# Optimization experiments

Hardware: AMD Instinct MI355X
Metric: run time of the kernel (lower is better)

## Reference

```python
import jax, jax.numpy as jnp
import numpy as np

N_HIDDEN = 512

def _lstm_cell(x, h, c, W_ih, W_hh, b):
    # PyTorch LSTMCell: gates ordered i, f, g, o
    gates = x @ W_ih.T + h @ W_hh.T + b  # [B, 4H]
    i, f, g, o = jnp.split(gates, 4, axis=-1)
    i = jax.nn.sigmoid(i)
    f = jax.nn.sigmoid(f)
    g = jnp.tanh(g)
    o = jax.nn.sigmoid(o)
    c_new = f * c + i * g
    h_new = o * jnp.tanh(c_new)
    return h_new, c_new

def setup_inputs() -> dict:
    key = jax.random.key(0)
    ks = jax.random.split(key, 10)
    B, T, H = 256, 1024, N_HIDDEN
    s1 = 1.0 / np.sqrt(H)
    inp = {
        'x': jax.random.normal(ks[0], (B, T), dtype=jnp.float32),
        'W_ih1': jax.random.uniform(ks[1], (4 * H, 1), jnp.float32, -s1, s1),
        'W_hh1': jax.random.uniform(ks[2], (4 * H, H), jnp.float32, -s1, s1),
        'b1': jax.random.uniform(ks[3], (4 * H,), jnp.float32, -s1, s1),
        'W_ih2': jax.random.uniform(ks[4], (4 * H, H), jnp.float32, -s1, s1),
        'W_hh2': jax.random.uniform(ks[5], (4 * H, H), jnp.float32, -s1, s1),
        'b2': jax.random.uniform(ks[6], (4 * H,), jnp.float32, -s1, s1),
        'W_lin': jax.random.uniform(ks[7], (1, H), jnp.float32, -s1, s1),
        'b_lin': jax.random.uniform(ks[8], (1,), jnp.float32, -s1, s1),
    }
    return inp

def reference(x, W_ih1, W_hh1, b1, W_ih2, W_hh2, b2, W_lin, b_lin):
    B, T = x.shape
    H = W_hh1.shape[1]
    zeros = jnp.zeros((B, H), dtype=x.dtype)
    init = (zeros, zeros, zeros, zeros)
    xs = x.T[:, :, None]  # [T, B, 1]

    def step(carry, x_t):
        h1, c1, h2, c2 = carry
        h1, c1 = _lstm_cell(x_t, h1, c1, W_ih1, W_hh1, b1)
        h2, c2 = _lstm_cell(h1, h2, c2, W_ih2, W_hh2, b2)
        out = h2 @ W_lin.T + b_lin  # [B, 1]
        return (h1, c1, h2, c2), out

    _, outs = jax.lax.scan(step, init, xs)  # outs: [T, B, 1]
    return outs[:, :, 0].T  # [B, T]
```

## Files before the change

### kernel.cpp

```cpp
#include <hip/hip_runtime.h>
#include <math.h>

#define BB   256
#define TT   1024
#define HH   512
#define NWG  256
#define NTHR 512
#define SLOT (HH*BB)
#define PADX 20

typedef _Float16 f16;
typedef _Float16 f16x8 __attribute__((ext_vector_type(8)));
typedef float    f32x4 __attribute__((ext_vector_type(4)));
typedef unsigned int u32;
typedef u32 u32x2 __attribute__((ext_vector_type(2)));
typedef unsigned short u16;
typedef unsigned char u8;

__device__ __forceinline__ f32x4 mf(f16x8 a, f16x8 b, f32x4 c){
  return __builtin_amdgcn_mfma_f32_16x16x32_f16(a, b, c, 0, 0, 0);
}

__device__ __forceinline__ float fast_sigmoid(float v){
  float e = __expf(-v);
  return __builtin_amdgcn_rcpf(1.0f + e);
}
__device__ __forceinline__ float fast_tanh(float v){
  float a = fabsf(v);
  float e = __expf(-2.0f * a);
  float r = (1.0f - e) * __builtin_amdgcn_rcpf(1.0f + e);
  return copysignf(r, v);
}

__device__ __forceinline__ void split_h(float hv, u16& hb, u8& lb){
  const f16 hh = (f16)hv;
  const f16 lh = (f16)((hv - (float)hh) * 2048.0f);
  union {f16 f; u16 u;} ch, cl; ch.f = hh; cl.f = lh;
  hb = ch.u;
  lb = (u8)(((u32)cl.u + 0x80u) >> 8);
}
__device__ __forceinline__ float join_h(u16 hb, u8 lb){
  union {u16 u; f16 f;} h, l;
  h.u = hb; l.u = (u16)((u32)lb << 8);
  return (float)h.f + (float)l.f * (1.0f/2048.0f);
}
__device__ __forceinline__ void st_wt_u16(u16* p, u16 v){
  __hip_atomic_store(p, v, __ATOMIC_RELAXED, __HIP_MEMORY_SCOPE_AGENT);
}
__device__ __forceinline__ void st_wt_u8(u8* p, u8 v){
  __hip_atomic_store(p, v, __ATOMIC_RELAXED, __HIP_MEMORY_SCOPE_AGENT);
}
__device__ __forceinline__ void st_wt_f32(float* p, float v){
  __hip_atomic_store(p, v, __ATOMIC_RELAXED, __HIP_MEMORY_SCOPE_AGENT);
}

__device__ __forceinline__ void build_hl(const u16* ph_, const u8* pl_, f16x8& fh, f16x8& fl){
  union {u32x2 d; u32 u[2];} ha, hb2;
  ha.d  = *(const u32x2*)ph_;
  hb2.d = *(const u32x2*)(ph_ + 1024);
  const u32 l0 = *(const u32*)pl_;
  const u32 l1 = *(const u32*)(pl_ + 1024);
  union {u32 u[4]; f16x8 f;} H, L;
  H.u[0]=ha.u[0]; H.u[1]=ha.u[1]; H.u[2]=hb2.u[0]; H.u[3]=hb2.u[1];
  L.u[0] = __builtin_amdgcn_perm(l0, 0u, 0x05010400u);
  L.u[1] = __builtin_amdgcn_perm(l0, 0u, 0x07010600u);
  L.u[2] = __builtin_amdgcn_perm(l1, 0u, 0x05010400u);
  L.u[3] = __builtin_amdgcn_perm(l1, 0u, 0x07010600u);
  fh = H.f; fl = L.f;
}

__device__ __forceinline__ void gridbar_g(unsigned* barb, unsigned ph){
  __syncthreads();
  if (threadIdx.x == 0){
    __builtin_amdgcn_fence(__ATOMIC_RELEASE, "agent");
    const unsigned g = blockIdx.x & 31u;
    unsigned old = __hip_atomic_fetch_add(&barb[g*16], 1u, __ATOMIC_RELAXED, __HIP_MEMORY_SCOPE_AGENT);
    if (old + 1u == 8u*ph){
      unsigned om = __hip_atomic_fetch_add(&barb[512], 1u, __ATOMIC_RELAXED, __HIP_MEMORY_SCOPE_AGENT);
      if (om + 1u == 32u*ph){
        #pragma unroll
        for (int r = 0; r < 32; ++r)
          __hip_atomic_store(&barb[544 + r*16], ph, __ATOMIC_RELAXED, __HIP_MEMORY_SCOPE_AGENT);
      }
    }
    while (__hip_atomic_load(&barb[544 + g*16], __ATOMIC_RELAXED, __HIP_MEMORY_SCOPE_AGENT) < ph){
      __builtin_amdgcn_s_sleep(2);
    }
    __builtin_amdgcn_fence(__ATOMIC_ACQUIRE, "agent");
  }
  __syncthreads();
}

__global__ __launch_bounds__(NTHR, 2) void lstm_mfma(
    const float* __restrict__ x,      const float* __restrict__ W_ih1,
    const float* __restrict__ W_hh1,  const float* __restrict__ b1,
    const float* __restrict__ W_ih2,  const float* __restrict__ W_hh2,
    const float* __restrict__ b2,     const float* __restrict__ W_lin,
    const float* __restrict__ b_lin,  float* __restrict__ out,
    char* __restrict__ wsb)
{
  __shared__ f16x8 A2hi[2048], A2lo[2048], A1hi[1024], A1lo[1024];
  __shared__ float xch[8][16*PADX];
  __shared__ float wlin_s[512];
  __shared__ float outpart[2][8];

  unsigned* bar = (unsigned*)wsb;
  float* xT = (float*)(wsb + 16384);
  u16* h1h = (u16*)(wsb + 16384 + 1048576);
  u8*  h1l = (u8*) ((char*)h1h + 4*SLOT);
  u16* h2h = (u16*)((char*)h1l + 2*SLOT);
  u8*  h2l = (u8*) ((char*)h2h + 4*SLOT);

  const int w   = blockIdx.x,  tid = threadIdx.x;
  const int l   = tid & 63,    wv  = tid >> 6;
  const int quad = l >> 4,     lc  = l & 15;
  const int p = w >> 1, cb = w & 1;
  const int j0 = 4*p;
  const int bcol = cb*128 + wv*16 + lc;
  const int jq = j0 + quad;
  const int b_out = cb*128 + p;
  unsigned* dbar = bar + cb*1024;
  unsigned* gbar = bar + 2048;
  const unsigned grp = (unsigned)(p >> 3);
  const int qrot = p & 3;

  {
    const int g_ = lc >> 2, jj_ = lc & 3;
    const int wrow = g_*HH + j0 + jj_;
    const float* rowI  = W_ih2 + (size_t)wrow*HH;
    const float* rowH2 = W_hh2 + (size_t)wrow*HH;
    const float* rowH1 = W_hh1 + (size_t)wrow*HH;
    for (int c = wv; c < 32; c += 8){
      const int kb = c*32 + quad*8;
      union {f16x8 v; f16 e[8];} hi8, lo8;
      #pragma unroll
      for (int i = 0; i < 8; ++i){
        const int k = kb + i;
        const float wval = (k < HH) ? rowI[k] : rowH2[k - HH];
        const f16 h_ = (f16)wval;
        hi8.e[i] = h_;
        lo8.e[i] = (f16)((wval - (float)h_) * 2048.0f);
      }
      A2hi[c*64 + l] = hi8.v;
      A2lo[c*64 + l] = lo8.v;
    }
    for (int c = wv; c < 16; c += 8){
      const int kb = c*32 + quad*8;
      union {f16x8 v; f16 e[8];} hi8, lo8;
      #pragma unroll
      for (int i = 0; i < 8; ++i){
        const float wval = rowH1[kb + i];
        const f16 h_ = (f16)wval;
        hi8.e[i] = h_;
        lo8.e[i] = (f16)((wval - (float)h_) * 2048.0f);
      }
      A1hi[c*64 + l] = hi8.v;
      A1lo[c*64 + l] = lo8.v;
    }
  }
  float wih1r[4], b1r[4], b2r[4];
  #pragma unroll
  for (int g = 0; g < 4; ++g){
    wih1r[g] = W_ih1[g*HH + jq];
    b1r[g]   = b1[g*HH + jq];
    b2r[g]   = b2[g*HH + jq];
  }
  const float blin = b_lin[0];
  wlin_s[tid] = W_lin[tid];

  {
    const int gid = w*NTHR + tid;
    #pragma unroll
    for (int i2 = 0; i2 < 2; ++i2){
      const int idx = gid + i2*131072;
      const int bb2 = idx >> 10, tt2 = idx & (TT-1);
      xT[(size_t)tt2*BB + bb2] = x[idx];
    }
  }
  {
    const int idx = w >> 1;
    const int off = SLOT + idx*1024 + (cb*128 + (tid & 127))*4 + (tid >> 7);
    st_wt_u16(&h2h[off], (u16)0);
    st_wt_u8 (&h2l[off], (u8)0);
  }

  gridbar_g(gbar, 1);

  float c1, c2 = 0.0f;
  {
    const float xv0 = xT[bcol];
    const float gi = fast_sigmoid(fmaf(xv0, wih1r[0], b1r[0]));
    const float gg = fast_tanh   (fmaf(xv0, wih1r[2], b1r[2]));
    const float go = fast_sigmoid(fmaf(xv0, wih1r[3], b1r[3]));
    c1 = gi * gg;
    const float hv = go * fast_tanh(c1);
    u16 hb; u8 lb; split_h(hv, hb, lb);
    const int off = p*1024 + bcol*4 + quad;
    st_wt_u16(&h1h[off], hb);
    st_wt_u8 (&h1l[off], lb);
  }
  gridbar_g(gbar, 2);

  for (int t = 0; t < TT; ++t){
    const int sR1 = ( t    & 1)*SLOT;
    const int sR2 = ((t+1) & 1)*SLOT;
    const int sW1 = ((t+1) & 1)*SLOT;
    const int sW2 = ( t    & 1)*SLOT;

    f32x4 aA2 = {0,0,0,0}, aB2 = {0,0,0,0}, aA1 = {0,0,0,0}, aB1 = {0,0,0,0};
    const u16* q1h = h1h + sR1 + quad*2048 + bcol*4;
    const u8*  q1l = h1l + sR1 + quad*2048 + bcol*4;
    const u16* q2h = h2h + sR2 + quad*2048 + bcol*4;
    const u8*  q2l = h2l + sR2 + quad*2048 + bcol*4;

    auto consume_chunk = [&](int c){
      f16x8 bh, bl;
      build_hl(q1h + c*8192, q1l + c*8192, bh, bl);
      const f16x8 a2h = A2hi[c*64 + l];
      const f16x8 a2l = A2lo[c*64 + l];
      const f16x8 a1h = A1hi[c*64 + l];
      const f16x8 a1l = A1lo[c*64 + l];
      aA2 = mf(a2h, bh, aA2);
      aB2 = mf(a2h, bl, aB2);
      aB2 = mf(a2l, bh, aB2);
      aA1 = mf(a1h, bh, aA1);
      aB1 = mf(a1h, bl, aB1);
      aB1 = mf(a1l, bh, aB1);
      f16x8 ch, cl;
      build_hl(q2h + c*8192, q2l + c*8192, ch, cl);
      const f16x8 d2h = A2hi[(c+16)*64 + l];
      const f16x8 d2l = A2lo[(c+16)*64 + l];
      aA2 = mf(d2h, ch, aA2);
      aB2 = mf(d2h, cl, aB2);
      aB2 = mf(d2l, ch, aB2);
    };

    const unsigned need = 8u * (unsigned)t;
    auto poll_mask = [&]() -> unsigned {
      unsigned cv = __hip_atomic_load(&dbar[(l & 15) * 16], __ATOMIC_RELAXED, __HIP_MEMORY_SCOPE_AGENT);
      return (unsigned)__ballot(cv >= need) & 0xFFFFu;
    };

    unsigned got = 0xFFFFu;
    if (t > 0) got = poll_mask();
    asm volatile("" ::: "memory");
    if (got == 0xFFFFu){
      #pragma unroll
      for (int i = 0; i < 16; ++i) consume_chunk((i + 4*qrot) & 15);
    } else {
      #pragma unroll
      for (int q = 0; q < 4; ++q){
        const int c0 = ((qrot + q) & 3) * 4;
        const unsigned qm = 0xFu << c0;
        while ((got & qm) != qm){
          __builtin_amdgcn_s_sleep(1);
          got |= poll_mask();
        }
        asm volatile("" ::: "memory");
        consume_chunk(c0 + 0);
        consume_chunk(c0 + 1);
        consume_chunk(c0 + 2);
        consume_chunk(c0 + 3);
      }
    }
    asm volatile("" ::: "memory");

    const int oidx = sR2 + (tid>>2)*1024 + b_out*4 + (tid&3);
    float opart = join_h(h2h[oidx], h2l[oidx]) * wlin_s[tid];

    float* xw = &xch[wv][0];
    {
      f32x4 pre;
      #pragma unroll
      for (int i = 0; i < 4; ++i) pre[i] = fmaf(aB2[i], 1.0f/2048.0f, aA2[i]);
      *(f32x4*)&xw[lc*PADX + quad*4] = pre;
      __threadfence_block();
      const float g0 = xw[lc*PADX + 0*4 + quad];
      const float g1 = xw[lc*PADX + 1*4 + quad];
      const float g2 = xw[lc*PADX + 2*4 + quad];
      const float g3 = xw[lc*PADX + 3*4 + quad];
      const float gi = fast_sigmoid(g0 + b2r[0]);
      const float gf = fast_sigmoid(g1 + b2r[1]);
      const float gg = fast_tanh   (g2 + b2r[2]);
      const float go = fast_sigmoid(g3 + b2r[3]);
      c2 = fmaf(gf, c2, gi*gg);
      const float hv = go * fast_tanh(c2);
      u16 hb; u8 lb; split_h(hv, hb, lb);
      const int off = sW2 + p*1024 + bcol*4 + quad;
      st_wt_u16(&h2h[off], hb);
      st_wt_u8 (&h2l[off], lb);
    }
    {
      f32x4 pre;
      #pragma unroll
      for (int i = 0; i < 4; ++i) pre[i] = fmaf(aB1[i], 1.0f/2048.0f, aA1[i]);
      __threadfence_block();
      *(f32x4*)&xw[lc*PADX + quad*4] = pre;
      __threadfence_block();
      const float g0 = xw[lc*PADX + 0*4 + quad];
      const float g1 = xw[lc*PADX + 1*4 + quad];
      const float g2 = xw[lc*PADX + 2*4 + quad];
      const float g3 = xw[lc*PADX + 3*4 + quad];
      const int tx = (t+1 < TT) ? (t+1) : (TT-1);
      const float xv = xT[(size_t)tx*BB + bcol];
      const float gi = fast_sigmoid(g0 + fmaf(xv, wih1r[0], b1r[0]));
      const float gf = fast_sigmoid(g1 + fmaf(xv, wih1r[1], b1r[1]));
      const float gg = fast_tanh   (g2 + fmaf(xv, wih1r[2], b1r[2]));
      const float go = fast_sigmoid(g3 + fmaf(xv, wih1r[3], b1r[3]));
      c1 = fmaf(gf, c1, gi*gg);
      const float hv = go * fast_tanh(c1);
      u16 hb; u8 lb; split_h(hv, hb, lb);
      const int off = sW1 + p*1024 + bcol*4 + quad;
      st_wt_u16(&h1h[off], hb);
      st_wt_u8 (&h1l[off], lb);
    }
    #pragma unroll
    for (int off = 32; off > 0; off >>= 1) opart += __shfl_down(opart, off, 64);
    if (l == 0) outpart[t & 1][wv] = opart;

    __syncthreads();
    if (tid == 0){
      __builtin_amdgcn_fence(__ATOMIC_RELEASE, "workgroup");
      __hip_atomic_fetch_add(&dbar[grp*16], 1u, __ATOMIC_RELAXED, __HIP_MEMORY_SCOPE_AGENT);
      __builtin_amdgcn_fence(__ATOMIC_ACQUIRE, "agent");
      if (t > 0){
        float s = blin;
        #pragma unroll
        for (int q2i = 0; q2i < 8; ++q2i) s += outpart[t & 1][q2i];
        st_wt_f32(&out[(size_t)b_out*TT + (t-1)], s);
      }
    }
    __syncthreads();
  }

  {
    const unsigned needT = 8u * (unsigned)TT;
    unsigned gotT = (unsigned)__ballot(
        __hip_atomic_load(&dbar[(l & 15) * 16], __ATOMIC_RELAXED, __HIP_MEMORY_SCOPE_AGENT) >= needT) & 0xFFFFu;
    while (gotT != 0xFFFFu){
      __builtin_amdgcn_s_sleep(1);
      gotT |= (unsigned)__ballot(
          __hip_atomic_load(&dbar[(l & 15) * 16], __ATOMIC_RELAXED, __HIP_MEMORY_SCOPE_AGENT) >= needT) & 0xFFFFu;
    }
    asm volatile("" ::: "memory");

    const int oidx = ((TT-1)&1)*SLOT + (tid>>2)*1024 + b_out*4 + (tid&3);
    float opart = join_h(h2h[oidx], h2l[oidx]) * wlin_s[tid];
    #pragma unroll
    for (int off = 32; off > 0; off >>= 1) opart += __shfl_down(opart, off, 64);
    if (l == 0) outpart[0][wv] = opart;
    __syncthreads();
    if (tid == 0){
      float s = blin;
      #pragma unroll
      for (int q2i = 0; q2i < 8; ++q2i) s += outpart[0][q2i];
      st_wt_f32(&out[(size_t)b_out*TT + (TT-1)], s);
    }
  }
}

extern "C" void kernel_launch(void* const* d_in, const int* in_sizes, int n_in,
                              void* d_out, int out_size, void* d_ws, size_t ws_size,
                              hipStream_t stream) {
  const float* x     = (const float*)d_in[0];
  const float* W_ih1 = (const float*)d_in[1];
  const float* W_hh1 = (const float*)d_in[2];
  const float* b1    = (const float*)d_in[3];
  const float* W_ih2 = (const float*)d_in[4];
  const float* W_hh2 = (const float*)d_in[5];
  const float* b2    = (const float*)d_in[6];
  const float* W_lin = (const float*)d_in[7];
  const float* b_lin = (const float*)d_in[8];
  float* out = (float*)d_out;
  char* wsb  = (char*)d_ws;

  hipMemsetAsync(d_ws, 0, 16384, stream);

  hipLaunchKernelGGL(lstm_mfma, dim3(NWG), dim3(NTHR), 0, stream,
                     x, W_ih1, W_hh1, b1, W_ih2, W_hh2, b2, W_lin, b_lin, out, wsb);
}
```

Before: 12.70 ms.

## Widen hidden-state layout and software-pipeline chunk loads ahead of MFMA compute

```diff
diff --git a/kernel.cpp b/kernel.cpp
--- a/kernel.cpp
+++ b/kernel.cpp
@@ -14,6 +14,7 @@
 typedef float    f32x4 __attribute__((ext_vector_type(4)));
 typedef unsigned int u32;
 typedef u32 u32x2 __attribute__((ext_vector_type(2)));
+typedef u32 u32x4 __attribute__((ext_vector_type(4)));
 typedef unsigned short u16;
 typedef unsigned char u8;
 
@@ -54,20 +55,17 @@
   __hip_atomic_store(p, v, __ATOMIC_RELAXED, __HIP_MEMORY_SCOPE_AGENT);
 }
 
-__device__ __forceinline__ void build_hl(const u16* ph_, const u8* pl_, f16x8& fh, f16x8& fl){
-  union {u32x2 d; u32 u[2];} ha, hb2;
-  ha.d  = *(const u32x2*)ph_;
-  hb2.d = *(const u32x2*)(ph_ + 1024);
-  const u32 l0 = *(const u32*)pl_;
-  const u32 l1 = *(const u32*)(pl_ + 1024);
+__device__ __forceinline__ void build2(u32x4 hd, u32x2 ld2, f16x8& fh, f16x8& fl){
   union {u32 u[4]; f16x8 f;} H, L;
-  H.u[0]=ha.u[0]; H.u[1]=ha.u[1]; H.u[2]=hb2.u[0]; H.u[3]=hb2.u[1];
-  L.u[0] = __builtin_amdgcn_perm(l0, 0u, 0x05010400u);
-  L.u[1] = __builtin_amdgcn_perm(l0, 0u, 0x07010600u);
-  L.u[2] = __builtin_amdgcn_perm(l1, 0u, 0x05010400u);
-  L.u[3] = __builtin_amdgcn_perm(l1, 0u, 0x07010600u);
+  H.u[0]=hd[0]; H.u[1]=hd[1]; H.u[2]=hd[2]; H.u[3]=hd[3];
+  L.u[0] = __builtin_amdgcn_perm(ld2[0], 0u, 0x05010400u);
+  L.u[1] = __builtin_amdgcn_perm(ld2[0], 0u, 0x07010600u);
+  L.u[2] = __builtin_amdgcn_perm(ld2[1], 0u, 0x05010400u);
+  L.u[3] = __builtin_amdgcn_perm(ld2[1], 0u, 0x07010600u);
   fh = H.f; fl = L.f;
 }
+
+struct St { u32x4 h1h4; u32x2 h1l2; u32x4 h2h4; u32x2 h2l2; };
 
 __device__ __forceinline__ void gridbar_g(unsigned* barb, unsigned ph){
   __syncthreads();
@@ -123,6 +121,7 @@
   unsigned* gbar = bar + 2048;
   const unsigned grp = (unsigned)(p >> 3);
   const int qrot = p & 3;
+  const int hoff = (p>>1)*2048 + bcol*8 + (p&1)*4 + quad;
 
   {
     const int g_ = lc >> 2, jj_ = lc & 3;
@@ -178,10 +177,9 @@
     }
   }
   {
-    const int idx = w >> 1;
-    const int off = SLOT + idx*1024 + (cb*128 + (tid & 127))*4 + (tid >> 7);
-    st_wt_u16(&h2h[off], (u16)0);
-    st_wt_u8 (&h2l[off], (u8)0);
+    const int idx = w*NTHR + tid;
+    st_wt_u16(&h2h[SLOT + idx], (u16)0);
+    st_wt_u8 (&h2l[SLOT + idx], (u8)0);
   }
 
   gridbar_g(gbar, 1);
@@ -195,27 +193,50 @@
     c1 = gi * gg;
     const float hv = go * fast_tanh(c1);
     u16 hb; u8 lb; split_h(hv, hb, lb);
-    const int off = p*1024 + bcol*4 + quad;
-    st_wt_u16(&h1h[off], hb);
-    st_wt_u8 (&h1l[off], lb);
+    st_wt_u16(&h1h[hoff], hb);
+    st_wt_u8 (&h1l[hoff], lb);
   }
   gridbar_g(gbar, 2);
+
+  auto poll_mask = [&](unsigned need) -> unsigned {
+    unsigned cv = __hip_atomic_load(&dbar[(l & 15) * 16], __ATOMIC_RELAXED, __HIP_MEMORY_SCOPE_AGENT);
+    return (unsigned)__ballot(cv >= need) & 0xFFFFu;
+  };
+
+  unsigned got = 0xFFFFu;
 
   for (int t = 0; t < TT; ++t){
     const int sR1 = ( t    & 1)*SLOT;
     const int sR2 = ((t+1) & 1)*SLOT;
     const int sW1 = ((t+1) & 1)*SLOT;
     const int sW2 = ( t    & 1)*SLOT;
+    const unsigned need = 8u * (unsigned)t;
 
     f32x4 aA2 = {0,0,0,0}, aB2 = {0,0,0,0}, aA1 = {0,0,0,0}, aB1 = {0,0,0,0};
-    const u16* q1h = h1h + sR1 + quad*2048 + bcol*4;
-    const u8*  q1l = h1l + sR1 + quad*2048 + bcol*4;
-    const u16* q2h = h2h + sR2 + quad*2048 + bcol*4;
-    const u8*  q2l = h2l + sR2 + quad*2048 + bcol*4;
-
-    auto consume_chunk = [&](int c){
+    const u16* q1h = h1h + sR1 + quad*2048 + bcol*8;
+    const u8*  q1l = h1l + sR1 + quad*2048 + bcol*8;
+    const u16* q2h = h2h + sR2 + quad*2048 + bcol*8;
+    const u8*  q2l = h2l + sR2 + quad*2048 + bcol*8;
+
+    auto waitq = [&](int qq){
+      const unsigned qm = 0xFu << (4*qq);
+      while ((got & qm) != qm){
+        __builtin_amdgcn_s_sleep(1);
+        got |= poll_mask(need);
+      }
+      asm volatile("" ::: "memory");
+    };
+    auto ldc = [&](int c) -> St {
+      St s;
+      s.h1h4 = *(const u32x4*)(q1h + c*8192);
+      s.h1l2 = *(const u32x2*)(q1l + c*8192);
+      s.h2h4 = *(const u32x4*)(q2h + c*8192);
+      s.h2l2 = *(const u32x2*)(q2l + c*8192);
+      return s;
+    };
+    auto cmp = [&](const St& s, int c){
       f16x8 bh, bl;
-      build_hl(q1h + c*8192, q1l + c*8192, bh, bl);
+      build2(s.h1h4, s.h1l2, bh, bl);
       const f16x8 a2h = A2hi[c*64 + l];
       const f16x8 a2l = A2lo[c*64 + l];
       const f16x8 a1h = A1hi[c*64 + l];
@@ -226,46 +247,34 @@
       aA1 = mf(a1h, bh, aA1);
       aB1 = mf(a1h, bl, aB1);
       aB1 = mf(a1l, bh, aB1);
-      f16x8 ch, cl;
-      build_hl(q2h + c*8192, q2l + c*8192, ch, cl);
+      f16x8 ch, cl2;
+      build2(s.h2h4, s.h2l2, ch, cl2);
       const f16x8 d2h = A2hi[(c+16)*64 + l];
       const f16x8 d2l = A2lo[(c+16)*64 + l];
       aA2 = mf(d2h, ch, aA2);
-      aB2 = mf(d2h, cl, aB2);
+      aB2 = mf(d2h, cl2, aB2);
       aB2 = mf(d2l, ch, aB2);
     };
 
-    const unsigned need = 8u * (unsigned)t;
-    auto poll_mask = [&]() -> unsigned {
-      unsigned cv = __hip_atomic_load(&dbar[(l & 15) * 16], __ATOMIC_RELAXED, __HIP_MEMORY_SCOPE_AGENT);
-      return (unsigned)__ballot(cv >= need) & 0xFFFFu;
-    };
-
-    unsigned got = 0xFFFFu;
-    if (t > 0) got = poll_mask();
-    asm volatile("" ::: "memory");
-    if (got == 0xFFFFu){
-      #pragma unroll
-      for (int i = 0; i < 16; ++i) consume_chunk((i + 4*qrot) & 15);
-    } else {
-      #pragma unroll
-      for (int q = 0; q < 4; ++q){
-        const int c0 = ((qrot + q) & 3) * 4;
-        const unsigned qm = 0xFu << c0;
-        while ((got & qm) != qm){
-          __builtin_amdgcn_s_sleep(1);
-          got |= poll_mask();
-        }
-        asm volatile("" ::: "memory");
-        consume_chunk(c0 + 0);
-        consume_chunk(c0 + 1);
-        consume_chunk(c0 + 2);
-        consume_chunk(c0 + 3);
-      }
-    }
-    asm volatile("" ::: "memory");
-
-    const int oidx = sR2 + (tid>>2)*1024 + b_out*4 + (tid&3);
+    const int cq0 = 4*qrot;
+    const int cq1 = 4*((qrot+1)&3);
+    const int cq2 = 4*((qrot+2)&3);
+    const int cq3 = 4*((qrot+3)&3);
+    St SA0,SA1,SA2,SA3, SB0,SB1,SB2,SB3;
+    waitq(cq0 >> 2);
+    SA0=ldc(cq0+0); SA1=ldc(cq0+1); SA2=ldc(cq0+2); SA3=ldc(cq0+3);
+    waitq(cq1 >> 2);
+    SB0=ldc(cq1+0); SB1=ldc(cq1+1); SB2=ldc(cq1+2); SB3=ldc(cq1+3);
+    cmp(SA0,cq0+0); cmp(SA1,cq0+1); cmp(SA2,cq0+2); cmp(SA3,cq0+3);
+    waitq(cq2 >> 2);
+    SA0=ldc(cq2+0); SA1=ldc(cq2+1); SA2=ldc(cq2+2); SA3=ldc(cq2+3);
+    cmp(SB0,cq1+0); cmp(SB1,cq1+1); cmp(SB2,cq1+2); cmp(SB3,cq1+3);
+    waitq(cq3 >> 2);
+    SB0=ldc(cq3+0); SB1=ldc(cq3+1); SB2=ldc(cq3+2); SB3=ldc(cq3+3);
+    cmp(SA0,cq2+0); cmp(SA1,cq2+1); cmp(SA2,cq2+2); cmp(SA3,cq2+3);
+    cmp(SB0,cq3+0); cmp(SB1,cq3+1); cmp(SB2,cq3+2); cmp(SB3,cq3+3);
+
+    const int oidx = sR2 + (tid>>3)*2048 + b_out*8 + (tid&7);
     float opart = join_h(h2h[oidx], h2l[oidx]) * wlin_s[tid];
 
     float* xw = &xch[wv][0];
@@ -286,9 +295,8 @@
       c2 = fmaf(gf, c2, gi*gg);
       const float hv = go * fast_tanh(c2);
       u16 hb; u8 lb; split_h(hv, hb, lb);
-      const int off = sW2 + p*1024 + bcol*4 + quad;
-      st_wt_u16(&h2h[off], hb);
-      st_wt_u8 (&h2l[off], lb);
+      st_wt_u16(&h2h[sW2 + hoff], hb);
+      st_wt_u8 (&h2l[sW2 + hoff], lb);
     }
     {
       f32x4 pre;
@@ -310,9 +318,8 @@
       c1 = fmaf(gf, c1, gi*gg);
       const float hv = go * fast_tanh(c1);
       u16 hb; u8 lb; split_h(hv, hb, lb);
-      const int off = sW1 + p*1024 + bcol*4 + quad;
-      st_wt_u16(&h1h[off], hb);
-      st_wt_u8 (&h1l[off], lb);
+      st_wt_u16(&h1h[sW1 + hoff], hb);
+      st_wt_u8 (&h1l[sW1 + hoff], lb);
     }
     #pragma unroll
     for (int off = 32; off > 0; off >>= 1) opart += __shfl_down(opart, off, 64);
@@ -330,21 +337,19 @@
         st_wt_f32(&out[(size_t)b_out*TT + (t-1)], s);
       }
     }
+    got = poll_mask(8u * (unsigned)(t+1));
     __syncthreads();
   }
 
   {
     const unsigned needT = 8u * (unsigned)TT;
-    unsigned gotT = (unsigned)__ballot(
-        __hip_atomic_load(&dbar[(l & 15) * 16], __ATOMIC_RELAXED, __HIP_MEMORY_SCOPE_AGENT) >= needT) & 0xFFFFu;
-    while (gotT != 0xFFFFu){
+    while (got != 0xFFFFu){
       __builtin_amdgcn_s_sleep(1);
-      gotT |= (unsigned)__ballot(
-          __hip_atomic_load(&dbar[(l & 15) * 16], __ATOMIC_RELAXED, __HIP_MEMORY_SCOPE_AGENT) >= needT) & 0xFFFFu;
+      got |= poll_mask(needT);
     }
     asm volatile("" ::: "memory");
 
-    const int oidx = ((TT-1)&1)*SLOT + (tid>>2)*1024 + b_out*4 + (tid&3);
+    const int oidx = ((TT-1)&1)*SLOT + (tid>>3)*2048 + b_out*8 + (tid&7);
     float opart = join_h(h2h[oidx], h2l[oidx]) * wlin_s[tid];
     #pragma unroll
     for (int off = 32; off > 0; off >>= 1) opart += __shfl_down(opart, off, 64);
```

After: 12.15 ms. 1.05x faster.
